# Kernel optimization log

Hardware: AMD Instinct MI355X
Metric: run time of the kernel (lower is better)

The kernel has to match this reference:

```python
import jax, jax.numpy as jnp
import numpy as np

WH, WW = 7, 7
DIM, HEADS = 256, 8


def make_table_index(wh, ww):
    # relative coords table (log-spaced CPB input) and relative position index
    ch = np.arange(-(wh - 1), wh, dtype=np.float32)
    cw = np.arange(-(ww - 1), ww, dtype=np.float32)
    t = np.stack(np.meshgrid(ch, cw, indexing='ij'), axis=-1)[None]  # [1,2wh-1,2ww-1,2]
    t = t.copy()
    t[..., 0] /= (wh - 1)
    t[..., 1] /= (ww - 1)
    t *= 8.0
    t = np.sign(t) * np.log2(np.abs(t) + 1.0) / np.log2(8.0)
    coords = np.stack(np.meshgrid(np.arange(wh), np.arange(ww), indexing='ij'))
    cf = coords.reshape(2, -1)
    rc = (cf[:, :, None] - cf[:, None, :]).transpose(1, 2, 0).copy()  # [N,N,2]
    rc[..., 0] += wh - 1
    rc[..., 1] += ww - 1
    rc[..., 0] *= 2 * ww - 1
    idx = rc.sum(-1)
    return t.astype(np.float32), idx.astype(np.int32)


def setup_inputs() -> dict:
    key = jax.random.key(0)
    ks = jax.random.split(key, 10)
    B_, N, C, H = 2048, WH * WW, DIM, HEADS
    table, idx = make_table_index(WH, WW)
    return {
        'x': jax.random.normal(ks[0], (B_, N, C), jnp.float32),
        'mask': jnp.zeros((64, N, N), jnp.float32),
        'qkv_w': jax.random.normal(ks[1], (3 * C, C), jnp.float32) * 0.02,
        'q_bias': jnp.zeros((C,), jnp.float32),
        'v_bias': jnp.zeros((C,), jnp.float32),
        'logit_scale': jnp.full((H, 1, 1), np.log(10.0), jnp.float32),
        'cpb_w1': jax.random.normal(ks[2], (512, 2), jnp.float32) * 0.02,
        'cpb_b1': jnp.zeros((512,), jnp.float32),
        'cpb_w2': jax.random.normal(ks[3], (H, 512), jnp.float32) * 0.02,
        'proj_w': jax.random.normal(ks[4], (C, C), jnp.float32) * 0.02,
        'proj_b': jnp.zeros((C,), jnp.float32),
        'rel_coords_table': jnp.asarray(table),
        'rel_pos_index': jnp.asarray(idx),
    }


def _l2norm(t):
    return t / jnp.maximum(jnp.linalg.norm(t, axis=-1, keepdims=True), 1e-12)


def reference(x, mask, qkv_w, q_bias, v_bias, logit_scale, cpb_w1, cpb_b1,
              cpb_w2, proj_w, proj_b, rel_coords_table, rel_pos_index):
    B_, N, C = x.shape
    H = logit_scale.shape[0]
    hd = C // H
    qkv_b = jnp.concatenate([q_bias, jnp.zeros_like(v_bias), v_bias])
    qkv = (x @ qkv_w.T + qkv_b).reshape(B_, N, 3, H, hd).transpose(2, 0, 3, 1, 4)
    q, k, v = qkv[0], qkv[1], qkv[2]  # [B_,H,N,hd]
    attn = jnp.einsum('bhnd,bhmd->bhnm', _l2norm(q), _l2norm(k))
    scale = jnp.exp(jnp.minimum(logit_scale, jnp.log(jnp.float32(100.0))))  # [H,1,1]
    attn = attn * scale[None]
    # CPB MLP -> relative position bias
    table = jax.nn.relu(rel_coords_table @ cpb_w1.T + cpb_b1) @ cpb_w2.T  # [1,Th,Tw,H]
    table = table.reshape(-1, H)
    bias = table[rel_pos_index.reshape(-1)].reshape(N, N, H).transpose(2, 0, 1)
    attn = attn + 16.0 * jax.nn.sigmoid(bias)[None]
    nW = mask.shape[0]
    attn = attn.reshape(B_ // nW, nW, H, N, N) + mask[None, :, None]
    attn = jax.nn.softmax(attn.reshape(B_, H, N, N), axis=-1)
    out = jnp.einsum('bhnm,bhmd->bhnd', attn, v).transpose(0, 2, 1, 3).reshape(B_, N, C)
    return out @ proj_w.T + proj_b
```

## Files before the change

### kernel.cpp

```cpp
#include <hip/hip_runtime.h>

#define DEV __device__ __forceinline__

typedef float  f32x4  __attribute__((ext_vector_type(4)));
typedef __bf16 bf16x8 __attribute__((ext_vector_type(8)));

DEV unsigned short f2bf(float f) {
  unsigned u = __float_as_uint(f);
  u += 0x7fffu + ((u >> 16) & 1u);
  return (unsigned short)(u >> 16);
}
DEV float bf2f(unsigned short v) { return __uint_as_float(((unsigned)v) << 16); }

DEV void cp16(const void* g, void* l) {
  __builtin_amdgcn_global_load_lds((const __attribute__((address_space(1))) void*)g,
                                   (__attribute__((address_space(3))) void*)l, 16, 0, 0);
}

__global__ __launch_bounds__(256) void prep_kernel(
    const float* __restrict__ qkv_w, const float* __restrict__ proj_w,
    const float* __restrict__ q_bias, const float* __restrict__ v_bias,
    unsigned short* __restrict__ wq, unsigned short* __restrict__ wp,
    float* __restrict__ qkvb)
{
  int gid = blockIdx.x * 256 + threadIdx.x;
  if (gid < 196608) wq[gid] = f2bf(qkv_w[gid]);
  else              wp[gid - 196608] = f2bf(proj_w[gid - 196608]);
  if (gid < 768)
    qkvb[gid] = (gid < 256) ? q_bias[gid] : ((gid < 512) ? 0.f : v_bias[gid - 512]);
}

__global__ __launch_bounds__(64) void cpb_mlp(
    const float* __restrict__ tab, const float* __restrict__ w1,
    const float* __restrict__ b1, const float* __restrict__ w2,
    float* __restrict__ table16)
{
  int r = blockIdx.x;
  int t = threadIdx.x;
  float x0 = tab[r * 2 + 0], x1 = tab[r * 2 + 1];
  float part[8];
#pragma unroll
  for (int h = 0; h < 8; ++h) part[h] = 0.f;
  for (int j = t; j < 512; j += 64) {
    float hv = fmaxf(w1[j * 2 + 0] * x0 + w1[j * 2 + 1] * x1 + b1[j], 0.f);
#pragma unroll
    for (int h = 0; h < 8; ++h) part[h] += hv * w2[h * 512 + j];
  }
#pragma unroll
  for (int h = 0; h < 8; ++h) {
    float v = part[h];
    for (int off = 32; off > 0; off >>= 1) v += __shfl_down(v, off, 64);
    if (t == 0) table16[r * 8 + h] = 16.f / (1.f + expf(-v));
  }
}

__global__ __launch_bounds__(256) void bmb(
    const float* __restrict__ t16, const int* __restrict__ ridx,
    const float* __restrict__ mask, float* __restrict__ bias64,
    float* __restrict__ mask64)
{
  int gid = blockIdx.x * 256 + threadIdx.x;
  int p = gid & 4095, i = p >> 6, j = p & 63;
  bool valid = (i < 49) && (j < 49);
  if (gid < 32768) {
    int h = gid >> 12;
    bias64[gid] = valid ? t16[ridx[i * 49 + j] * 8 + h] : 0.f;
  } else {
    int g2 = gid - 32768;
    int w = g2 >> 12;
    mask64[g2] = valid ? mask[w * 2401 + i * 49 + j] : 0.f;
  }
}

__global__ __launch_bounds__(256) void gemm_qkv(
    const float* __restrict__ X, const unsigned short* __restrict__ W,
    const float* __restrict__ bias, unsigned short* __restrict__ qkv)
{
  __shared__ __align__(1024) unsigned short sA[128 * 64];
  __shared__ __align__(1024) unsigned short sB[128 * 64];
  const int t = threadIdx.x, w = t >> 6, l = t & 63, quad = l >> 4, l15 = l & 15;
  const int idx = blockIdx.x;
  const int x8 = idx & 7, local = idx >> 3;
  const int my = x8 * 98 + local / 6, bnb = local % 6;
  const int bm = my * 128, bn = bnb * 128;
  const int wm = (w >> 1) * 64, wn = (w & 1) * 64;
  const int arow = t >> 1, ahalf = t & 1;
  const int srow = t >> 3, sch = t & 7;

  f32x4 acc[4][4] = {};
#pragma unroll 1
  for (int kt = 0; kt < 4; ++kt) {
    const int k0 = kt << 6;
    if (kt) __syncthreads();
#pragma unroll
    for (int i = 0; i < 4; ++i) {
      const int row = i * 32 + srow;
      const int sc  = sch ^ (srow & 7);
      cp16(W + (size_t)(bn + row) * 256 + k0 + sc * 8, sB + (i * 256 + w * 64) * 8);
    }
    {
      const float* ap = X + (size_t)(bm + arow) * 256 + k0 + ahalf * 32;
#pragma unroll
      for (int c = 0; c < 4; ++c) {
        float4 f0 = *(const float4*)(ap + c * 8);
        float4 f1 = *(const float4*)(ap + c * 8 + 4);
        uint4 u;
        u.x = f2bf(f0.x) | ((unsigned)f2bf(f0.y) << 16);
        u.y = f2bf(f0.z) | ((unsigned)f2bf(f0.w) << 16);
        u.z = f2bf(f1.x) | ((unsigned)f2bf(f1.y) << 16);
        u.w = f2bf(f1.z) | ((unsigned)f2bf(f1.w) << 16);
        const int cb = ahalf * 4 + c;
        *(uint4*)&sA[arow * 64 + ((cb ^ (arow & 7)) * 8)] = u;
      }
    }
    __syncthreads();
#pragma unroll
    for (int kk = 0; kk < 2; ++kk) {
      bf16x8 af[4], bfr[4];
#pragma unroll
      for (int mt = 0; mt < 4; ++mt)
        af[mt] = *(const bf16x8*)&sA[(wm + mt * 16 + l15) * 64 + (((4 * kk + quad) ^ (l15 & 7)) * 8)];
#pragma unroll
      for (int nt = 0; nt < 4; ++nt)
        bfr[nt] = *(const bf16x8*)&sB[(wn + nt * 16 + l15) * 64 + (((4 * kk + quad) ^ (l15 & 7)) * 8)];
#pragma unroll
      for (int mt = 0; mt < 4; ++mt)
#pragma unroll
        for (int nt = 0; nt < 4; ++nt)
          acc[mt][nt] = __builtin_amdgcn_mfma_f32_16x16x32_bf16(af[mt], bfr[nt], acc[mt][nt], 0, 0, 0);
    }
  }
  unsigned bq[16]; int tq[16];
#pragma unroll
  for (int mt = 0; mt < 4; ++mt)
#pragma unroll
    for (int r = 0; r < 4; ++r) {
      const int row = bm + wm + mt * 16 + quad * 4 + r;
      const unsigned bb = (unsigned)(((unsigned long long)row * 87652394ull) >> 32);
      bq[mt * 4 + r] = bb;
      tq[mt * 4 + r] = row - (int)bb * 49;
    }
#pragma unroll
  for (int nt = 0; nt < 4; ++nt) {
    const int col0 = bn + wn + nt * 16;
    const int s = col0 >> 8, h = (col0 >> 5) & 7, dbase = col0 & 31;
    const int d = dbase + l15;
    const float bv = bias[col0 + l15];
#pragma unroll
    for (int mt = 0; mt < 4; ++mt)
#pragma unroll
      for (int r = 0; r < 4; ++r) {
        const unsigned bb = bq[mt * 4 + r];
        const int tok = tq[mt * 4 + r];
        qkv[(size_t)((bb * 8u + h) * 3u + s) * 1568 + tok * 32 + d] =
            f2bf(acc[mt][nt][r] + bv);
      }
  }
}

__global__ __launch_bounds__(256) void attn2(
    const unsigned short* __restrict__ qkv, const float* __restrict__ logit_scale,
    const float* __restrict__ bias64, const float* __restrict__ mask64,
    unsigned short* __restrict__ aout)
{
  __shared__ __align__(1024) char smem[4 * 12544];
  const int w = threadIdx.x >> 6, l = threadIdx.x & 63, quad = l >> 4, l15 = l & 15;
  const int flat = blockIdx.x * 4 + w;
  const int b = flat >> 3, h = flat & 7;
  char* my = smem + w * 12544;
  unsigned short* vT = (unsigned short*)my;
  unsigned short* P  = (unsigned short*)(my + 4096);
  float* rk = (float*)(my + 12288);

  const unsigned short* qb = qkv + (size_t)flat * 4704;
  const unsigned short* kb = qb + 1568;
  const unsigned short* vb = qb + 3136;

  bf16x8 kf[4], qf[4];
#pragma unroll
  for (int mt = 0; mt < 4; ++mt) kf[mt] = *(const bf16x8*)(kb + (mt * 16 + l15) * 32 + quad * 8);
#pragma unroll
  for (int nt = 0; nt < 4; ++nt) qf[nt] = *(const bf16x8*)(qb + (nt * 16 + l15) * 32 + quad * 8);

  const float scale = __expf(fminf(logit_scale[h], 4.60517019f));
  float rqv[4];
#pragma unroll
  for (int nt = 0; nt < 4; ++nt) {
    float s = 0.f;
#pragma unroll
    for (int d = 0; d < 8; ++d) { float f = (float)qf[nt][d]; s += f * f; }
    s += __shfl_xor(s, 16, 64); s += __shfl_xor(s, 32, 64);
    rqv[nt] = scale / fmaxf(sqrtf(s), 1e-12f);
  }
#pragma unroll
  for (int mt = 0; mt < 4; ++mt) {
    float s = 0.f;
#pragma unroll
    for (int d = 0; d < 8; ++d) { float f = (float)kf[mt][d]; s += f * f; }
    s += __shfl_xor(s, 16, 64); s += __shfl_xor(s, 32, 64);
    if (quad == 0) rk[mt * 16 + l15] = 1.f / fmaxf(sqrtf(s), 1e-12f);
  }

  if (l < 49) {
    unsigned short vv[32];
#pragma unroll
    for (int c = 0; c < 4; ++c) *(uint4*)&vv[c * 8] = *(const uint4*)(vb + l * 32 + c * 8);
#pragma unroll
    for (int d = 0; d < 32; ++d)
      vT[d * 64 + (((l >> 3) ^ (d & 7)) << 3) + (l & 7)] = vv[d];
  } else {
#pragma unroll
    for (int d = 0; d < 32; ++d)
      vT[d * 64 + (((l >> 3) ^ (d & 7)) << 3) + (l & 7)] = 0;
  }
  __syncthreads();

  f32x4 acc[4][4] = {};
#pragma unroll
  for (int mt = 0; mt < 4; ++mt)
#pragma unroll
    for (int nt = 0; nt < 4; ++nt)
      acc[mt][nt] = __builtin_amdgcn_mfma_f32_16x16x32_bf16(kf[mt], qf[nt], acc[mt][nt], 0, 0, 0);

  const float* bh = bias64 + (size_t)h * 4096;
  const float* mw = mask64 + (size_t)(b & 63) * 4096;
#pragma unroll
  for (int nt = 0; nt < 4; ++nt) {
    const int i = nt * 16 + l15;
    const float rqi = rqv[nt];
    float s[4][4];
    float mx = -1e30f;
#pragma unroll
    for (int mt = 0; mt < 4; ++mt) {
      const int jb = mt * 16 + quad * 4;
      const f32x4 b4  = *(const f32x4*)(bh + i * 64 + jb);
      const f32x4 m4  = *(const f32x4*)(mw + i * 64 + jb);
      const f32x4 rk4 = *(const f32x4*)(rk + jb);
#pragma unroll
      for (int r = 0; r < 4; ++r) {
        float sv = acc[mt][nt][r] * (rqi * rk4[r]) + b4[r] + m4[r];
        sv = (jb + r < 49) ? sv : -1e30f;
        s[mt][r] = sv;
        mx = fmaxf(mx, sv);
      }
    }
    mx = fmaxf(mx, __shfl_xor(mx, 16, 64));
    mx = fmaxf(mx, __shfl_xor(mx, 32, 64));
    float sum = 0.f;
    float p[4][4];
#pragma unroll
    for (int mt = 0; mt < 4; ++mt)
#pragma unroll
      for (int r = 0; r < 4; ++r) {
        float pv = __expf(s[mt][r] - mx);
        p[mt][r] = pv; sum += pv;
      }
    sum += __shfl_xor(sum, 16, 64);
    sum += __shfl_xor(sum, 32, 64);
    const float rs = 1.f / sum;
#pragma unroll
    for (int mt = 0; mt < 4; ++mt) {
      unsigned d0 = f2bf(p[mt][0] * rs) | ((unsigned)f2bf(p[mt][1] * rs) << 16);
      unsigned d1 = f2bf(p[mt][2] * rs) | ((unsigned)f2bf(p[mt][3] * rs) << 16);
      const int c = 2 * mt + (quad >> 1);
      uint2 uv; uv.x = d0; uv.y = d1;
      *(uint2*)((char*)P + i * 128 + ((c ^ (i & 7)) * 16) + (quad & 1) * 8) = uv;
    }
  }
  __syncthreads();

  f32x4 oacc[2][4] = {};
#pragma unroll
  for (int kk = 0; kk < 2; ++kk) {
    bf16x8 vf[2], pf[4];
#pragma unroll
    for (int mt = 0; mt < 2; ++mt)
      vf[mt] = *(const bf16x8*)((char*)vT + (mt * 16 + l15) * 128 + (((4 * kk + quad) ^ (l15 & 7)) * 16));
#pragma unroll
    for (int nt = 0; nt < 4; ++nt)
      pf[nt] = *(const bf16x8*)((char*)P + (nt * 16 + l15) * 128 + (((4 * kk + quad) ^ (l15 & 7)) * 16));
#pragma unroll
    for (int mt = 0; mt < 2; ++mt)
#pragma unroll
      for (int nt = 0; nt < 4; ++nt)
        oacc[mt][nt] = __builtin_amdgcn_mfma_f32_16x16x32_bf16(vf[mt], pf[nt], oacc[mt][nt], 0, 0, 0);
  }

#pragma unroll
  for (int nt = 0; nt < 4; ++nt) {
    const int tok = nt * 16 + l15;
    if (tok < 49) {
      unsigned short* op = aout + (size_t)(b * 49 + tok) * 256 + h * 32;
#pragma unroll
      for (int mt = 0; mt < 2; ++mt) {
        unsigned u0 = f2bf(oacc[mt][nt][0]) | ((unsigned)f2bf(oacc[mt][nt][1]) << 16);
        unsigned u1 = f2bf(oacc[mt][nt][2]) | ((unsigned)f2bf(oacc[mt][nt][3]) << 16);
        uint2 uv; uv.x = u0; uv.y = u1;
        *(uint2*)(op + mt * 16 + quad * 4) = uv;
      }
    }
  }
}

template <bool OBF16>
__global__ __launch_bounds__(256) void gemm128(
    const unsigned short* __restrict__ A, const unsigned short* __restrict__ W,
    const float* __restrict__ bias, void* __restrict__ Yp, int N, int K)
{
  __shared__ __align__(1024) unsigned short sA[128 * 64];
  __shared__ __align__(1024) unsigned short sB[128 * 64];
  const int t = threadIdx.x, w = t >> 6, l = t & 63, quad = l >> 4, l15 = l & 15;
  const int bm = blockIdx.y * 128, bn = blockIdx.x * 128;
  const int wm = (w >> 1) * 64, wn = (w & 1) * 64;
  const int srow = t >> 3, sch = t & 7;

  f32x4 acc[4][4] = {};
  const int KT = K >> 6;
  for (int kt = 0; kt < KT; ++kt) {
    const int k0 = kt << 6;
    if (kt) __syncthreads();
#pragma unroll
    for (int i = 0; i < 4; ++i) {
      const int row = i * 32 + srow;
      const int sc  = sch ^ (srow & 7);
      cp16(A + (size_t)(bm + row) * K + k0 + sc * 8, sA + (i * 256 + w * 64) * 8);
      cp16(W + (size_t)(bn + row) * K + k0 + sc * 8, sB + (i * 256 + w * 64) * 8);
    }
    __syncthreads();
#pragma unroll
    for (int kk = 0; kk < 2; ++kk) {
      bf16x8 af[4], bfr[4];
#pragma unroll
      for (int mt = 0; mt < 4; ++mt)
        af[mt] = *(const bf16x8*)&sA[(wm + mt * 16 + l15) * 64 + (((4 * kk + quad) ^ (l15 & 7)) * 8)];
#pragma unroll
      for (int nt = 0; nt < 4; ++nt)
        bfr[nt] = *(const bf16x8*)&sB[(wn + nt * 16 + l15) * 64 + (((4 * kk + quad) ^ (l15 & 7)) * 8)];
#pragma unroll
      for (int mt = 0; mt < 4; ++mt)
#pragma unroll
        for (int nt = 0; nt < 4; ++nt)
          acc[mt][nt] = __builtin_amdgcn_mfma_f32_16x16x32_bf16(af[mt], bfr[nt], acc[mt][nt], 0, 0, 0);
    }
  }
#pragma unroll
  for (int nt = 0; nt < 4; ++nt) {
    const int col = bn + wn + nt * 16 + l15;
    const float bv = bias[col];
#pragma unroll
    for (int mt = 0; mt < 4; ++mt) {
#pragma unroll
      for (int r = 0; r < 4; ++r) {
        const int row = bm + wm + mt * 16 + quad * 4 + r;
        float v = acc[mt][nt][r] + bv;
        if constexpr (OBF16) ((unsigned short*)Yp)[(size_t)row * N + col] = f2bf(v);
        else                 ((float*)Yp)[(size_t)row * N + col] = v;
      }
    }
  }
}

extern "C" void kernel_launch(void* const* d_in, const int* in_sizes, int n_in,
                              void* d_out, int out_size, void* d_ws, size_t ws_size,
                              hipStream_t stream) {
  const float* x           = (const float*)d_in[0];
  const float* mask        = (const float*)d_in[1];
  const float* qkv_w       = (const float*)d_in[2];
  const float* q_bias      = (const float*)d_in[3];
  const float* v_bias      = (const float*)d_in[4];
  const float* logit_scale = (const float*)d_in[5];
  const float* cpb_w1      = (const float*)d_in[6];
  const float* cpb_b1      = (const float*)d_in[7];
  const float* cpb_w2      = (const float*)d_in[8];
  const float* proj_w      = (const float*)d_in[9];
  const float* proj_b      = (const float*)d_in[10];
  const float* rel_tab     = (const float*)d_in[11];
  const int*   rel_idx     = (const int*)d_in[12];
  float*       out         = (float*)d_out;

  char* ws = (char*)d_ws;
  unsigned short* qkvp    = (unsigned short*)(ws + 0);
  unsigned short* aows    = (unsigned short*)(ws + 154140672);
  unsigned short* wq      = (unsigned short*)(ws + 205520896);
  unsigned short* wp      = (unsigned short*)(ws + 205914112);
  float*          qkvb    = (float*)(ws + 206045184);
  float*          table16 = (float*)(ws + 206048256);
  float*          bias64  = (float*)(ws + 206053888);
  float*          mask64  = (float*)(ws + 206184960);

  prep_kernel<<<1024, 256, 0, stream>>>(qkv_w, proj_w, q_bias, v_bias, wq, wp, qkvb);
  cpb_mlp<<<169, 64, 0, stream>>>(rel_tab, cpb_w1, cpb_b1, cpb_w2, table16);
  bmb<<<1152, 256, 0, stream>>>(table16, rel_idx, mask, bias64, mask64);
  gemm_qkv<<<4704, 256, 0, stream>>>(x, wq, qkvb, qkvp);
  attn2<<<4096, 256, 0, stream>>>(qkvp, logit_scale, bias64, mask64, aows);
  gemm128<false><<<dim3(2, 784), 256, 0, stream>>>(aows, wp, proj_b, out, 256, 256);
}
```

Measured before the change: 441.6 us.

## Swap MFMA operand order to vectorize GEMM epilogue stores, permuting head dims

```diff
diff --git a/kernel.cpp b/kernel.cpp
--- a/kernel.cpp
+++ b/kernel.cpp
@@ -116,45 +116,40 @@
     __syncthreads();
 #pragma unroll
     for (int kk = 0; kk < 2; ++kk) {
-      bf16x8 af[4], bfr[4];
+      bf16x8 xf[4], wf[4];
 #pragma unroll
       for (int mt = 0; mt < 4; ++mt)
-        af[mt] = *(const bf16x8*)&sA[(wm + mt * 16 + l15) * 64 + (((4 * kk + quad) ^ (l15 & 7)) * 8)];
-#pragma unroll
-      for (int nt = 0; nt < 4; ++nt)
-        bfr[nt] = *(const bf16x8*)&sB[(wn + nt * 16 + l15) * 64 + (((4 * kk + quad) ^ (l15 & 7)) * 8)];
-#pragma unroll
-      for (int mt = 0; mt < 4; ++mt)
-#pragma unroll
-        for (int nt = 0; nt < 4; ++nt)
-          acc[mt][nt] = __builtin_amdgcn_mfma_f32_16x16x32_bf16(af[mt], bfr[nt], acc[mt][nt], 0, 0, 0);
-    }
-  }
-  unsigned bq[16]; int tq[16];
-#pragma unroll
-  for (int mt = 0; mt < 4; ++mt)
-#pragma unroll
-    for (int r = 0; r < 4; ++r) {
-      const int row = bm + wm + mt * 16 + quad * 4 + r;
-      const unsigned bb = (unsigned)(((unsigned long long)row * 87652394ull) >> 32);
-      bq[mt * 4 + r] = bb;
-      tq[mt * 4 + r] = row - (int)bb * 49;
-    }
-#pragma unroll
-  for (int nt = 0; nt < 4; ++nt) {
-    const int col0 = bn + wn + nt * 16;
-    const int s = col0 >> 8, h = (col0 >> 5) & 7, dbase = col0 & 31;
-    const int d = dbase + l15;
-    const float bv = bias[col0 + l15];
-#pragma unroll
-    for (int mt = 0; mt < 4; ++mt)
-#pragma unroll
-      for (int r = 0; r < 4; ++r) {
-        const unsigned bb = bq[mt * 4 + r];
-        const int tok = tq[mt * 4 + r];
-        qkv[(size_t)((bb * 8u + h) * 3u + s) * 1568 + tok * 32 + d] =
-            f2bf(acc[mt][nt][r] + bv);
-      }
+        xf[mt] = *(const bf16x8*)&sA[(wm + mt * 16 + l15) * 64 + (((4 * kk + quad) ^ (l15 & 7)) * 8)];
+#pragma unroll
+      for (int nt = 0; nt < 4; ++nt)
+        wf[nt] = *(const bf16x8*)&sB[(wn + nt * 16 + l15) * 64 + (((4 * kk + quad) ^ (l15 & 7)) * 8)];
+#pragma unroll
+      for (int nt = 0; nt < 4; ++nt)
+#pragma unroll
+        for (int mt = 0; mt < 4; ++mt)
+          acc[nt][mt] = __builtin_amdgcn_mfma_f32_16x16x32_bf16(wf[nt], xf[mt], acc[nt][mt], 0, 0, 0);
+    }
+  }
+  const int nbase = bn + wn;
+#pragma unroll
+  for (int mA = 0; mA < 4; ++mA) {
+    const int mrow = bm + wm + mA * 16 + l15;
+    const unsigned bb = (unsigned)(((unsigned long long)mrow * 87652394ull) >> 32);
+    const int tok = mrow - (int)bb * 49;
+#pragma unroll
+    for (int k = 0; k < 2; ++k) {
+      const int n0 = nbase + k * 32;
+      const int s = n0 >> 8, h = (n0 >> 5) & 7;
+      const f32x4 b0 = *(const f32x4*)(bias + n0 + quad * 4);
+      const f32x4 b1 = *(const f32x4*)(bias + n0 + 16 + quad * 4);
+      const f32x4 a0 = acc[2 * k][mA], a1 = acc[2 * k + 1][mA];
+      uint4 u;
+      u.x = f2bf(a0[0] + b0[0]) | ((unsigned)f2bf(a0[1] + b0[1]) << 16);
+      u.y = f2bf(a0[2] + b0[2]) | ((unsigned)f2bf(a0[3] + b0[3]) << 16);
+      u.z = f2bf(a1[0] + b1[0]) | ((unsigned)f2bf(a1[1] + b1[1]) << 16);
+      u.w = f2bf(a1[2] + b1[2]) | ((unsigned)f2bf(a1[3] + b1[3]) << 16);
+      *(uint4*)(qkv + (size_t)((bb * 8u + h) * 3u + s) * 1568 + tok * 32 + quad * 8) = u;
+    }
   }
 }
 
@@ -206,8 +201,10 @@
 #pragma unroll
     for (int c = 0; c < 4; ++c) *(uint4*)&vv[c * 8] = *(const uint4*)(vb + l * 32 + c * 8);
 #pragma unroll
-    for (int d = 0; d < 32; ++d)
-      vT[d * 64 + (((l >> 3) ^ (d & 7)) << 3) + (l & 7)] = vv[d];
+    for (int dp = 0; dp < 32; ++dp) {
+      const int d = (((dp >> 2) & 1) << 4) + ((dp >> 3) << 2) + (dp & 3);
+      vT[d * 64 + (((l >> 3) ^ (d & 7)) << 3) + (l & 7)] = vv[dp];
+    }
   } else {
 #pragma unroll
     for (int d = 0; d < 32; ++d)
@@ -302,10 +299,9 @@
   }
 }
 
-template <bool OBF16>
-__global__ __launch_bounds__(256) void gemm128(
+__global__ __launch_bounds__(256) void gemm_proj(
     const unsigned short* __restrict__ A, const unsigned short* __restrict__ W,
-    const float* __restrict__ bias, void* __restrict__ Yp, int N, int K)
+    const float* __restrict__ bias, float* __restrict__ Y)
 {
   __shared__ __align__(1024) unsigned short sA[128 * 64];
   __shared__ __align__(1024) unsigned short sB[128 * 64];
@@ -315,47 +311,44 @@
   const int srow = t >> 3, sch = t & 7;
 
   f32x4 acc[4][4] = {};
-  const int KT = K >> 6;
-  for (int kt = 0; kt < KT; ++kt) {
+  for (int kt = 0; kt < 4; ++kt) {
     const int k0 = kt << 6;
     if (kt) __syncthreads();
 #pragma unroll
     for (int i = 0; i < 4; ++i) {
       const int row = i * 32 + srow;
       const int sc  = sch ^ (srow & 7);
-      cp16(A + (size_t)(bm + row) * K + k0 + sc * 8, sA + (i * 256 + w * 64) * 8);
-      cp16(W + (size_t)(bn + row) * K + k0 + sc * 8, sB + (i * 256 + w * 64) * 8);
+      cp16(A + (size_t)(bm + row) * 256 + k0 + sc * 8, sA + (i * 256 + w * 64) * 8);
+      cp16(W + (size_t)(bn + row) * 256 + k0 + sc * 8, sB + (i * 256 + w * 64) * 8);
     }
     __syncthreads();
 #pragma unroll
     for (int kk = 0; kk < 2; ++kk) {
-      bf16x8 af[4], bfr[4];
+      bf16x8 xf[4], wf[4];
 #pragma unroll
       for (int mt = 0; mt < 4; ++mt)
-        af[mt] = *(const bf16x8*)&sA[(wm + mt * 16 + l15) * 64 + (((4 * kk + quad) ^ (l15 & 7)) * 8)];
-#pragma unroll
-      for (int nt = 0; nt < 4; ++nt)
-        bfr[nt] = *(const bf16x8*)&sB[(wn + nt * 16 + l15) * 64 + (((4 * kk + quad) ^ (l15 & 7)) * 8)];
-#pragma unroll
-      for (int mt = 0; mt < 4; ++mt)
-#pragma unroll
-        for (int nt = 0; nt < 4; ++nt)
-          acc[mt][nt] = __builtin_amdgcn_mfma_f32_16x16x32_bf16(af[mt], bfr[nt], acc[mt][nt], 0, 0, 0);
-    }
-  }
-#pragma unroll
-  for (int nt = 0; nt < 4; ++nt) {
-    const int col = bn + wn + nt * 16 + l15;
-    const float bv = bias[col];
-#pragma unroll
-    for (int mt = 0; mt < 4; ++mt) {
-#pragma unroll
-      for (int r = 0; r < 4; ++r) {
-        const int row = bm + wm + mt * 16 + quad * 4 + r;
-        float v = acc[mt][nt][r] + bv;
-        if constexpr (OBF16) ((unsigned short*)Yp)[(size_t)row * N + col] = f2bf(v);
-        else                 ((float*)Yp)[(size_t)row * N + col] = v;
-      }
+        xf[mt] = *(const bf16x8*)&sA[(wm + mt * 16 + l15) * 64 + (((4 * kk + quad) ^ (l15 & 7)) * 8)];
+#pragma unroll
+      for (int nt = 0; nt < 4; ++nt)
+        wf[nt] = *(const bf16x8*)&sB[(wn + nt * 16 + l15) * 64 + (((4 * kk + quad) ^ (l15 & 7)) * 8)];
+#pragma unroll
+      for (int nt = 0; nt < 4; ++nt)
+#pragma unroll
+        for (int mt = 0; mt < 4; ++mt)
+          acc[nt][mt] = __builtin_amdgcn_mfma_f32_16x16x32_bf16(wf[nt], xf[mt], acc[nt][mt], 0, 0, 0);
+    }
+  }
+#pragma unroll
+  for (int mA = 0; mA < 4; ++mA) {
+    const int row = bm + wm + mA * 16 + l15;
+    float* orow = Y + (size_t)row * 256;
+#pragma unroll
+    for (int nW = 0; nW < 4; ++nW) {
+      const int c0 = bn + wn + nW * 16 + quad * 4;
+      const f32x4 bv = *(const f32x4*)(bias + c0);
+      f32x4 v = acc[nW][mA];
+      v[0] += bv[0]; v[1] += bv[1]; v[2] += bv[2]; v[3] += bv[3];
+      *(f32x4*)(orow + c0) = v;
     }
   }
 }
@@ -393,5 +386,5 @@
   bmb<<<1152, 256, 0, stream>>>(table16, rel_idx, mask, bias64, mask64);
   gemm_qkv<<<4704, 256, 0, stream>>>(x, wq, qkvb, qkvp);
   attn2<<<4096, 256, 0, stream>>>(qkvp, logit_scale, bias64, mask64, aows);
-  gemm128<false><<<dim3(2, 784), 256, 0, stream>>>(aows, wp, proj_b, out, 256, 256);
-}
+  gemm_proj<<<dim3(2, 784), 256, 0, stream>>>(aows, wp, proj_b, out);
+}
```

Measured after the change: 413.9 us. 1.07x faster.
